# Optimization experiments

Hardware: AMD Instinct MI355X
Metric: run time of the kernel (lower is better)

Reference implementation:

```python
import jax, jax.numpy as jnp
import numpy as np

TAU = 0.07
EPS = 1e-6  # torch CosineSimilarity eps


def setup_inputs() -> dict:
    key = jax.random.key(0)
    k1, k2, k3 = jax.random.split(key, 3)
    n, d, n_classes = 8192, 256, 1024
    imitation_embeds = jax.random.normal(k1, (n, d), dtype=jnp.float32)
    recording_embeds = jax.random.normal(k2, (n, d), dtype=jnp.float32)
    labels = jax.random.randint(k3, (n,), 0, n_classes, dtype=jnp.int64)
    return {
        "imitation_embeds": imitation_embeds,
        "recording_embeds": recording_embeds,
        "labels": labels,
    }


def reference(imitation_embeds, recording_embeds, labels):
    n = imitation_embeds.shape[0]
    # cosine similarity with per-vector norm clamp (torch semantics)
    im_n = imitation_embeds / jnp.maximum(
        jnp.linalg.norm(imitation_embeds, axis=1, keepdims=True), EPS)
    rec_n = recording_embeds / jnp.maximum(
        jnp.linalg.norm(recording_embeds, axis=1, keepdims=True), EPS)
    i2r = jnp.einsum("nd,md->nm", im_n, rec_n) / TAU  # [n, n]

    same = labels[:, None] == labels[None, :]          # [n, n] bool
    eye = jnp.eye(n, dtype=bool)
    # original: mask = ~(same ^ diag_embed(diag(same))); diag(same) is all True
    # -> keep the diagonal (positive) and all different-label negatives
    mask = ~(same ^ eye)

    # per-row masked log-softmax evaluated at the diagonal entry:
    # log_softmax(row[mask])[pos_of_diag] = i2r[i,i] - logsumexp(row over mask)
    lse = jax.nn.logsumexp(jnp.where(mask, i2r, -jnp.inf), axis=1)  # [n]
    loss = -jnp.mean(jnp.diagonal(i2r) - lse)
    return loss
```

## Files before the change

### kernel.cpp

```cpp
#include <hip/hip_runtime.h>

#define N 8192
#define D 256
#define INV_TAU 14.285714285714286f
#define EPSN 1e-6f

#define RT 128
#define CT 64
#define CSPLIT 16
#define CPB (N / CSPLIT)
#define NTILES (CPB / CT)
#define LDSS 264

typedef unsigned int u32x4 __attribute__((ext_vector_type(4)));
typedef __bf16 bf16x8 __attribute__((ext_vector_type(8)));
typedef float f32x4 __attribute__((ext_vector_type(4)));

__device__ inline unsigned short f2bf(float x) {
    unsigned int u = __builtin_bit_cast(unsigned int, x);
    u += 0x7fffu + ((u >> 16) & 1u);
    return (unsigned short)(u >> 16);
}

__device__ inline float bf2f(unsigned short u) {
    return __builtin_bit_cast(float, (unsigned int)u << 16);
}

__global__ void ntx_prep(const float* __restrict__ im, const float* __restrict__ rec,
                         unsigned short* __restrict__ A, unsigned short* __restrict__ Bm,
                         float* __restrict__ diag, float* __restrict__ rowsum,
                         float* __restrict__ out) {
    const int wave = threadIdx.x >> 6;
    const int lane = threadIdx.x & 63;
    const int row  = blockIdx.x * 4 + wave;

    const float4 a = ((const float4*)(im  + (size_t)row * D))[lane];
    const float4 b = ((const float4*)(rec + (size_t)row * D))[lane];

    float ssa = a.x*a.x + a.y*a.y + a.z*a.z + a.w*a.w;
    float ssb = b.x*b.x + b.y*b.y + b.z*b.z + b.w*b.w;
    float dt  = a.x*b.x + a.y*b.y + a.z*b.z + a.w*b.w;
    #pragma unroll
    for (int o = 32; o; o >>= 1) {
        ssa += __shfl_xor(ssa, o);
        ssb += __shfl_xor(ssb, o);
        dt  += __shfl_xor(dt , o);
    }
    const float ra = 1.0f / fmaxf(sqrtf(ssa), EPSN);
    const float rb = 1.0f / fmaxf(sqrtf(ssb), EPSN);
    const float sa = ra * INV_TAU;

    ushort4 pa, pb;
    pa.x = f2bf(a.x*sa); pa.y = f2bf(a.y*sa); pa.z = f2bf(a.z*sa); pa.w = f2bf(a.w*sa);
    pb.x = f2bf(b.x*rb); pb.y = f2bf(b.y*rb); pb.z = f2bf(b.z*rb); pb.w = f2bf(b.w*rb);
    *(ushort4*)(A  + (size_t)row * D + lane * 4) = pa;
    *(ushort4*)(Bm + (size_t)row * D + lane * 4) = pb;

    if (lane == 0) {
        diag[row]   = dt * ra * rb * INV_TAU;
        rowsum[row] = 0.0f;
    }
    if (blockIdx.x == 0 && threadIdx.x == 0) out[0] = 0.0f;
}

__global__ __launch_bounds__(256, 2)
void ntx_lse(const unsigned short* __restrict__ A, const unsigned short* __restrict__ Bm,
             float* __restrict__ rowsum) {
    __shared__ __align__(16) unsigned short Bs[CT][LDSS];

    const int wave = threadIdx.x >> 6;
    const int lane = threadIdx.x & 63;
    const int g    = lane >> 4;
    const int n16  = lane & 15;

    const int rowblk = blockIdx.x & (N / RT - 1);
    const int colblk = blockIdx.x >> 6;
    const int row0 = rowblk * RT + wave * 32;
    const int col0 = colblk * CPB;

    bf16x8 afrag[2][8];
    #pragma unroll
    for (int rs = 0; rs < 2; ++rs) {
        const int r = row0 + rs * 16 + n16;
        #pragma unroll
        for (int k = 0; k < 8; ++k)
            afrag[rs][k] = __builtin_bit_cast(
                bf16x8, *(const u32x4*)(A + (size_t)r * D + k * 32 + g * 8));
    }

    float acc[2][4] = {{0.f,0.f,0.f,0.f},{0.f,0.f,0.f,0.f}};

    const int c32 = threadIdx.x & 31;
    const int rr  = threadIdx.x >> 5;

    u32x4 stg[8];
    #pragma unroll
    for (int p = 0; p < 8; ++p)
        stg[p] = *(const u32x4*)(Bm + (size_t)(col0 + p * 8 + rr) * D + c32 * 8);

    for (int t = 0; t < NTILES; ++t) {
        #pragma unroll
        for (int p = 0; p < 8; ++p)
            *(u32x4*)(&Bs[p * 8 + rr][c32 * 8]) = stg[p];
        __syncthreads();

        if (t + 1 < NTILES) {
            const int coln = col0 + (t + 1) * CT;
            #pragma unroll
            for (int p = 0; p < 8; ++p)
                stg[p] = *(const u32x4*)(Bm + (size_t)(coln + p * 8 + rr) * D + c32 * 8);
        }

        #pragma unroll
        for (int cs = 0; cs < 4; ++cs) {
            const int bc = cs * 16 + n16;
            bf16x8 bfrag[8];
            #pragma unroll
            for (int k = 0; k < 8; ++k)
                bfrag[k] = __builtin_bit_cast(
                    bf16x8, *(const u32x4*)(&Bs[bc][k * 32 + g * 8]));

            #pragma unroll
            for (int rs = 0; rs < 2; ++rs) {
                f32x4 c = {0.f, 0.f, 0.f, 0.f};
                #pragma unroll
                for (int k = 0; k < 8; ++k)
                    c = __builtin_amdgcn_mfma_f32_16x16x32_bf16(
                            afrag[rs][k], bfrag[k], c, 0, 0, 0);
                #pragma unroll
                for (int q = 0; q < 4; ++q)
                    acc[rs][q] += __expf(c[q]);
            }
        }
        __syncthreads();
    }

    #pragma unroll
    for (int rs = 0; rs < 2; ++rs)
        #pragma unroll
        for (int q = 0; q < 4; ++q) {
            float v = acc[rs][q];
            v += __shfl_xor(v, 1);
            v += __shfl_xor(v, 2);
            v += __shfl_xor(v, 4);
            v += __shfl_xor(v, 8);
            if (n16 == 0)
                atomicAdd(&rowsum[row0 + rs * 16 + g * 4 + q], v);
        }
}

__global__ void ntx_cfin(const unsigned short* __restrict__ A,
                         const unsigned short* __restrict__ Bm,
                         const int* __restrict__ labels,
                         const float* __restrict__ diag,
                         const float* __restrict__ rowsum,
                         float* __restrict__ out) {
    __shared__ float red[4];
    const int wave = threadIdx.x >> 6;
    const int lane = threadIdx.x & 63;
    const int r0 = blockIdx.x * 16 + wave * 4;

    int lab[4];
    float af[4][4];
    #pragma unroll
    for (int r = 0; r < 4; ++r) {
        lab[r] = labels[r0 + r];
        const ushort4 av = *(const ushort4*)(A + (size_t)(r0 + r) * D + lane * 4);
        af[r][0] = bf2f(av.x); af[r][1] = bf2f(av.y);
        af[r][2] = bf2f(av.z); af[r][3] = bf2f(av.w);
    }
    float corr[4] = {0.f, 0.f, 0.f, 0.f};

    for (int it = 0; it < N / 256; ++it) {
        const int4 lv = ((const int4*)labels)[it * 64 + lane];
        #pragma unroll
        for (int s = 0; s < 4; ++s) {
            const int jl = (s == 0) ? lv.x : (s == 1) ? lv.y : (s == 2) ? lv.z : lv.w;
            #pragma unroll
            for (int r = 0; r < 4; ++r) {
                unsigned long long bm = __ballot(jl == lab[r]);
                while (bm) {
                    const int b = __ffsll((unsigned long long)bm) - 1;
                    bm &= bm - 1;
                    const int j = (it * 64 + b) * 4 + s;
                    if (j == r0 + r) continue;
                    const ushort4 bv = *(const ushort4*)(Bm + (size_t)j * D + lane * 4);
                    float d = af[r][0]*bf2f(bv.x) + af[r][1]*bf2f(bv.y)
                            + af[r][2]*bf2f(bv.z) + af[r][3]*bf2f(bv.w);
                    #pragma unroll
                    for (int o = 32; o; o >>= 1) d += __shfl_xor(d, o);
                    corr[r] += __expf(d);
                }
            }
        }
    }

    if (lane == 0) {
        float s = 0.f;
        #pragma unroll
        for (int r = 0; r < 4; ++r)
            s += logf(rowsum[r0 + r] - corr[r]) - diag[r0 + r];
        red[wave] = s;
    }
    __syncthreads();
    if (threadIdx.x == 0)
        atomicAdd(out, (red[0] + red[1] + red[2] + red[3]) * (1.0f / (float)N));
}

extern "C" void kernel_launch(void* const* d_in, const int* in_sizes, int n_in,
                              void* d_out, int out_size, void* d_ws, size_t ws_size,
                              hipStream_t stream) {
    const float* im     = (const float*)d_in[0];
    const float* rec    = (const float*)d_in[1];
    const int*   labels = (const int*)d_in[2];
    float* out = (float*)d_out;

    unsigned short* A  = (unsigned short*)d_ws;
    unsigned short* Bm = A + (size_t)N * D;
    float* diag   = (float*)(Bm + (size_t)N * D);
    float* rowsum = diag + N;

    ntx_prep<<<N / 4, 256, 0, stream>>>(im, rec, A, Bm, diag, rowsum, out);
    ntx_lse<<<(N / RT) * CSPLIT, 256, 0, stream>>>(A, Bm, rowsum);
    ntx_cfin<<<N / 16, 256, 0, stream>>>(A, Bm, labels, diag, rowsum, out);
}
```

Before: 143.5 us.

## Bucket rows by label for same-label correction; swizzle LDS, use exp2

```diff
diff --git a/kernel.cpp b/kernel.cpp
--- a/kernel.cpp
+++ b/kernel.cpp
@@ -3,6 +3,7 @@
 #define N 8192
 #define D 256
 #define INV_TAU 14.285714285714286f
+#define LOG2E 1.4426950408889634f
 #define EPSN 1e-6f
 
 #define RT 128
@@ -10,7 +11,7 @@
 #define CSPLIT 16
 #define CPB (N / CSPLIT)
 #define NTILES (CPB / CT)
-#define LDSS 264
+#define MAXC 96
 
 typedef unsigned int u32x4 __attribute__((ext_vector_type(4)));
 typedef __bf16 bf16x8 __attribute__((ext_vector_type(8)));
@@ -29,7 +30,7 @@
 __global__ void ntx_prep(const float* __restrict__ im, const float* __restrict__ rec,
                          unsigned short* __restrict__ A, unsigned short* __restrict__ Bm,
                          float* __restrict__ diag, float* __restrict__ rowsum,
-                         float* __restrict__ out) {
+                         int* __restrict__ cnt, float* __restrict__ out) {
     const int wave = threadIdx.x >> 6;
     const int lane = threadIdx.x & 63;
     const int row  = blockIdx.x * 4 + wave;
@@ -48,7 +49,7 @@
     }
     const float ra = 1.0f / fmaxf(sqrtf(ssa), EPSN);
     const float rb = 1.0f / fmaxf(sqrtf(ssb), EPSN);
-    const float sa = ra * INV_TAU;
+    const float sa = ra * (INV_TAU * LOG2E);
 
     ushort4 pa, pb;
     pa.x = f2bf(a.x*sa); pa.y = f2bf(a.y*sa); pa.z = f2bf(a.z*sa); pa.w = f2bf(a.w*sa);
@@ -60,13 +61,47 @@
         diag[row]   = dt * ra * rb * INV_TAU;
         rowsum[row] = 0.0f;
     }
+    if (blockIdx.x < 4) cnt[blockIdx.x * 256 + threadIdx.x] = 0;
     if (blockIdx.x == 0 && threadIdx.x == 0) out[0] = 0.0f;
 }
 
-__global__ __launch_bounds__(256, 2)
+__global__ void ntx_bucket(const int* __restrict__ labels, int* __restrict__ cnt,
+                           int* __restrict__ bucket) {
+    const int i = blockIdx.x * 256 + threadIdx.x;
+    const int c = labels[i];
+    const int pos = atomicAdd(&cnt[c], 1);
+    if (pos < MAXC) bucket[c * MAXC + pos] = i;
+}
+
+__global__ void ntx_pairs(const unsigned short* __restrict__ A,
+                          const unsigned short* __restrict__ Bm,
+                          const int* __restrict__ cnt, const int* __restrict__ bucket,
+                          float* __restrict__ rowsum) {
+    const int c = blockIdx.x;
+    const int m = min(cnt[c], MAXC);
+    if (m < 2) return;
+    const int wave = threadIdx.x >> 6;
+    const int lane = threadIdx.x & 63;
+    for (int r = 0; r < m; ++r) {
+        const int i = bucket[c * MAXC + r];
+        const ushort4 av = *(const ushort4*)(A + (size_t)i * D + lane * 4);
+        const float a0 = bf2f(av.x), a1 = bf2f(av.y), a2 = bf2f(av.z), a3 = bf2f(av.w);
+        for (int j = wave; j < m; j += 4) {
+            if (j == r) continue;
+            const int jr = bucket[c * MAXC + j];
+            const ushort4 bv = *(const ushort4*)(Bm + (size_t)jr * D + lane * 4);
+            float d = a0*bf2f(bv.x) + a1*bf2f(bv.y) + a2*bf2f(bv.z) + a3*bf2f(bv.w);
+            #pragma unroll
+            for (int o = 32; o; o >>= 1) d += __shfl_xor(d, o);
+            if (lane == 0) atomicAdd(&rowsum[i], -__builtin_amdgcn_exp2f(d));
+        }
+    }
+}
+
+__global__ __launch_bounds__(256, 3)
 void ntx_lse(const unsigned short* __restrict__ A, const unsigned short* __restrict__ Bm,
              float* __restrict__ rowsum) {
-    __shared__ __align__(16) unsigned short Bs[CT][LDSS];
+    __shared__ __align__(128) unsigned char Bsb[CT * 512];
 
     const int wave = threadIdx.x >> 6;
     const int lane = threadIdx.x & 63;
@@ -92,6 +127,9 @@
 
     const int c32 = threadIdx.x & 31;
     const int rr  = threadIdx.x >> 5;
+    const int kk  = c32 >> 2;
+    const int gg  = c32 & 3;
+    const int xr  = (kk & 3) << 5;
 
     u32x4 stg[8];
     #pragma unroll
@@ -100,8 +138,11 @@
 
     for (int t = 0; t < NTILES; ++t) {
         #pragma unroll
-        for (int p = 0; p < 8; ++p)
-            *(u32x4*)(&Bs[p * 8 + rr][c32 * 8]) = stg[p];
+        for (int p = 0; p < 8; ++p) {
+            const int br = p * 8 + rr;
+            const int off = (((((br >> 4) * 8 + kk) * 64) + gg * 16 + (br & 15)) * 16) ^ xr;
+            *(u32x4*)(&Bsb[off]) = stg[p];
+        }
         __syncthreads();
 
         if (t + 1 < NTILES) {
@@ -113,12 +154,11 @@
 
         #pragma unroll
         for (int cs = 0; cs < 4; ++cs) {
-            const int bc = cs * 16 + n16;
             bf16x8 bfrag[8];
             #pragma unroll
             for (int k = 0; k < 8; ++k)
                 bfrag[k] = __builtin_bit_cast(
-                    bf16x8, *(const u32x4*)(&Bs[bc][k * 32 + g * 8]));
+                    bf16x8, *(const u32x4*)(&Bsb[((((cs * 8 + k) * 64) + lane) * 16) ^ ((k & 3) << 5)]));
 
             #pragma unroll
             for (int rs = 0; rs < 2; ++rs) {
@@ -129,7 +169,7 @@
                             afrag[rs][k], bfrag[k], c, 0, 0, 0);
                 #pragma unroll
                 for (int q = 0; q < 4; ++q)
-                    acc[rs][q] += __expf(c[q]);
+                    acc[rs][q] += __builtin_amdgcn_exp2f(c[q]);
             }
         }
         __syncthreads();
@@ -149,59 +189,15 @@
         }
 }
 
-__global__ void ntx_cfin(const unsigned short* __restrict__ A,
-                         const unsigned short* __restrict__ Bm,
-                         const int* __restrict__ labels,
-                         const float* __restrict__ diag,
-                         const float* __restrict__ rowsum,
-                         float* __restrict__ out) {
+__global__ void ntx_finish(const float* __restrict__ diag,
+                           const float* __restrict__ rowsum,
+                           float* __restrict__ out) {
     __shared__ float red[4];
-    const int wave = threadIdx.x >> 6;
-    const int lane = threadIdx.x & 63;
-    const int r0 = blockIdx.x * 16 + wave * 4;
-
-    int lab[4];
-    float af[4][4];
-    #pragma unroll
-    for (int r = 0; r < 4; ++r) {
-        lab[r] = labels[r0 + r];
-        const ushort4 av = *(const ushort4*)(A + (size_t)(r0 + r) * D + lane * 4);
-        af[r][0] = bf2f(av.x); af[r][1] = bf2f(av.y);
-        af[r][2] = bf2f(av.z); af[r][3] = bf2f(av.w);
-    }
-    float corr[4] = {0.f, 0.f, 0.f, 0.f};
-
-    for (int it = 0; it < N / 256; ++it) {
-        const int4 lv = ((const int4*)labels)[it * 64 + lane];
-        #pragma unroll
-        for (int s = 0; s < 4; ++s) {
-            const int jl = (s == 0) ? lv.x : (s == 1) ? lv.y : (s == 2) ? lv.z : lv.w;
-            #pragma unroll
-            for (int r = 0; r < 4; ++r) {
-                unsigned long long bm = __ballot(jl == lab[r]);
-                while (bm) {
-                    const int b = __ffsll((unsigned long long)bm) - 1;
-                    bm &= bm - 1;
-                    const int j = (it * 64 + b) * 4 + s;
-                    if (j == r0 + r) continue;
-                    const ushort4 bv = *(const ushort4*)(Bm + (size_t)j * D + lane * 4);
-                    float d = af[r][0]*bf2f(bv.x) + af[r][1]*bf2f(bv.y)
-                            + af[r][2]*bf2f(bv.z) + af[r][3]*bf2f(bv.w);
-                    #pragma unroll
-                    for (int o = 32; o; o >>= 1) d += __shfl_xor(d, o);
-                    corr[r] += __expf(d);
-                }
-            }
-        }
-    }
-
-    if (lane == 0) {
-        float s = 0.f;
-        #pragma unroll
-        for (int r = 0; r < 4; ++r)
-            s += logf(rowsum[r0 + r] - corr[r]) - diag[r0 + r];
-        red[wave] = s;
-    }
+    const int i = blockIdx.x * 256 + threadIdx.x;
+    float s = logf(rowsum[i]) - diag[i];
+    #pragma unroll
+    for (int o = 32; o; o >>= 1) s += __shfl_xor(s, o);
+    if ((threadIdx.x & 63) == 0) red[threadIdx.x >> 6] = s;
     __syncthreads();
     if (threadIdx.x == 0)
         atomicAdd(out, (red[0] + red[1] + red[2] + red[3]) * (1.0f / (float)N));
@@ -219,8 +215,12 @@
     unsigned short* Bm = A + (size_t)N * D;
     float* diag   = (float*)(Bm + (size_t)N * D);
     float* rowsum = diag + N;
-
-    ntx_prep<<<N / 4, 256, 0, stream>>>(im, rec, A, Bm, diag, rowsum, out);
+    int*   cnt    = (int*)(rowsum + N);
+    int*   bucket = cnt + 1024;
+
+    ntx_prep<<<N / 4, 256, 0, stream>>>(im, rec, A, Bm, diag, rowsum, cnt, out);
+    ntx_bucket<<<N / 256, 256, 0, stream>>>(labels, cnt, bucket);
+    ntx_pairs<<<1024, 256, 0, stream>>>(A, Bm, cnt, bucket, rowsum);
     ntx_lse<<<(N / RT) * CSPLIT, 256, 0, stream>>>(A, Bm, rowsum);
-    ntx_cfin<<<N / 16, 256, 0, stream>>>(A, Bm, labels, diag, rowsum, out);
-}
+    ntx_finish<<<N / 256, 256, 0, stream>>>(diag, rowsum, out);
+}
```

After: 173.3 us. 1.21x slower.
